# Performance work log

Hardware: AMD Instinct MI355X
Metric: run time of the kernel (lower is better)

The kernel has to match this reference:

```python
import jax, jax.numpy as jnp
import numpy as np

B = 65536          # batch
E = 512            # embedding_dim
SL = 128           # speed_latent_dim
H = 256            # hidden_size
NB = 6             # num_branch
D = E + SL         # 640, branch input dim


def _linear_init(k, din, dout):
    bound = 1.0 / np.sqrt(din)
    kw, kb = jax.random.split(k)
    W = jax.random.uniform(kw, (din, dout), minval=-bound, maxval=bound, dtype=jnp.float32)
    b = jax.random.uniform(kb, (dout,), minval=-bound, maxval=bound, dtype=jnp.float32)
    return W, b


def setup_inputs() -> dict:
    key = jax.random.key(0)
    ks = jax.random.split(key, 10)
    embedding = jax.random.normal(ks[0], (B, E), dtype=jnp.float32)
    speed = jax.random.uniform(ks[1], (B, 1), dtype=jnp.float32)
    command = jax.random.randint(ks[2], (B,), 1, NB + 1)  # values in 1..6

    # speed_in: Linear(1,H) -> ReLU -> Linear(H,SL)
    si_W1, si_b1 = _linear_init(ks[3], 1, H)
    si_W2, si_b2 = _linear_init(ks[4], H, SL)

    # speed_out: Linear(D,H) -> ReLU -> Linear(H,H) -> ReLU -> Linear(H,1)
    so_W1, so_b1 = _linear_init(ks[5], D, H)
    so_W2, so_b2 = _linear_init(ks[6], H, H)
    so_W3, so_b3 = _linear_init(ks[7], H, 1)

    # NB branches, each Linear(D,H)->ReLU->Linear(H,H)->ReLU->Linear(H,3)->Sigmoid
    def mk_branch(k):
        k1, k2, k3 = jax.random.split(k, 3)
        W1, b1 = _linear_init(k1, D, H)
        W2, b2 = _linear_init(k2, H, H)
        W3, b3 = _linear_init(k3, H, 3)
        return W1, b1, W2, b2, W3, b3

    bW1, bb1, bW2, bb2, bW3, bb3 = jax.vmap(mk_branch)(jax.random.split(ks[8], NB))

    return {
        "embedding": embedding, "speed": speed, "command": command,
        "si_W1": si_W1, "si_b1": si_b1, "si_W2": si_W2, "si_b2": si_b2,
        "bW1": bW1, "bb1": bb1, "bW2": bW2, "bb2": bb2, "bW3": bW3, "bb3": bb3,
        "so_W1": so_W1, "so_b1": so_b1, "so_W2": so_W2, "so_b2": so_b2,
        "so_W3": so_W3, "so_b3": so_b3,
    }


def reference(embedding, speed, command,
              si_W1, si_b1, si_W2, si_b2,
              bW1, bb1, bW2, bb2, bW3, bb3,
              so_W1, so_b1, so_W2, so_b2, so_W3, so_b3):
    # speed_in MLP and concat
    s = jax.nn.relu(speed @ si_W1 + si_b1) @ si_W2 + si_b2          # [B, SL]
    emb = jnp.concatenate([embedding, s], axis=1)                    # [B, D]

    # all branches computed densely (as in the torch module), then one-hot mask
    h1 = jax.nn.relu(jnp.einsum('bd,ndh->nbh', emb, bW1) + bb1[:, None, :])   # [NB,B,H]
    h2 = jax.nn.relu(jnp.einsum('nbh,nhk->nbk', h1, bW2) + bb2[:, None, :])   # [NB,B,H]
    out = jax.nn.sigmoid(jnp.einsum('nbk,nko->nbo', h2, bW3) + bb3[:, None, :])  # [NB,B,3]

    mask = (jnp.arange(NB)[:, None] == (command - 1)[None, :]).astype(out.dtype)  # [NB,B]
    control_pred = jnp.sum(out * mask[:, :, None], axis=0)           # [B, 3]

    # speed prediction head
    sp = jax.nn.relu(emb @ so_W1 + so_b1)
    sp = jax.nn.relu(sp @ so_W2 + so_b2)
    speed_pred = sp @ so_W3 + so_b3                                  # [B, 1]

    return control_pred, speed_pred
```

## Files before the change

kernel.cpp:

```cpp
#include <hip/hip_runtime.h>
#include <cstdint>
#include <cstddef>

typedef _Float16 f16;
typedef f16 f16x8 __attribute__((ext_vector_type(8)));
typedef float f32x4 __attribute__((ext_vector_type(4)));

#define B_ROWS 65536
#define TILE_M 128
#define NT_BRANCH 518
#define NT_SPEED 512
#define NWG_HEADS (NT_BRANCH + NT_SPEED)

constexpr size_t OFF_AF16   = 0;
constexpr size_t SZ_AF16    = (size_t)B_ROWS * 640 * 2;
constexpr size_t OFF_SIW2T  = OFF_AF16 + SZ_AF16;
constexpr size_t SZ_SIW2T   = (size_t)128 * 256 * 2;
constexpr size_t OFF_BW1T   = OFF_SIW2T + SZ_SIW2T;
constexpr size_t SZ_BW1T    = (size_t)6 * 256 * 640 * 2;
constexpr size_t OFF_BW2T   = OFF_BW1T + SZ_BW1T;
constexpr size_t SZ_BW2T    = (size_t)6 * 256 * 256 * 2;
constexpr size_t OFF_SOW1T  = OFF_BW2T + SZ_BW2T;
constexpr size_t SZ_SOW1T   = (size_t)256 * 640 * 2;
constexpr size_t OFF_SOW2T  = OFF_SOW1T + SZ_SOW1T;
constexpr size_t SZ_SOW2T   = (size_t)256 * 256 * 2;
constexpr size_t OFF_BW3T16 = OFF_SOW2T + SZ_SOW2T;
constexpr size_t SZ_BW3T16  = (size_t)6 * 16 * 256 * 2;
constexpr size_t OFF_SOW3T16= OFF_BW3T16 + SZ_BW3T16;
constexpr size_t SZ_SOW3T16 = (size_t)16 * 256 * 2;
constexpr size_t OFF_COUNTS = OFF_SOW3T16 + SZ_SOW3T16;
constexpr size_t OFF_CURSORS= OFF_COUNTS + 256;
constexpr size_t OFF_BINBASE= OFF_CURSORS + 256;
constexpr size_t OFF_TILECMD= OFF_BINBASE + 256;
constexpr size_t OFF_PERM   = OFF_TILECMD + 4352;
constexpr size_t WS_NEEDED  = OFF_PERM + (size_t)NT_BRANCH * TILE_M * 4;

#define MFMA16(a, b, c) __builtin_amdgcn_mfma_f32_16x16x32_f16(a, b, c, 0, 0, 0)
#define BARSYNC() asm volatile("s_waitcnt lgkmcnt(0)\n\ts_barrier" ::: "memory")

__global__ void prep_kernel(const float* __restrict__ emb,
                            const float* __restrict__ siW2,
                            const float* __restrict__ bW1,
                            const float* __restrict__ bW2,
                            const float* __restrict__ soW1,
                            const float* __restrict__ soW2,
                            const float* __restrict__ bW3,
                            const float* __restrict__ soW3,
                            f16* __restrict__ AF16,
                            f16* __restrict__ siW2T, f16* __restrict__ bW1T,
                            f16* __restrict__ bW2T, f16* __restrict__ soW1T,
                            f16* __restrict__ soW2T,
                            f16* __restrict__ bW3T16, f16* __restrict__ soW3T16,
                            int* __restrict__ counts, int* __restrict__ cursors,
                            int* __restrict__ perm)
{
    const int bx = blockIdx.x;
    const int tx = threadIdx.x, ty = threadIdx.y;
    const int tid = ty * 32 + tx;
    if (bx >= 1860) {
        const int cb = bx - 1860;
        const int wv = tid >> 6, ln = tid & 63;
        #pragma unroll
        for (int it = 0; it < 4; ++it) {
            const int row = cb * 16 + it * 4 + wv;
            const float* src = emb + (size_t)row * 512 + ln * 8;
            const float4 f0 = ((const float4*)src)[0];
            const float4 f1 = ((const float4*)src)[1];
            f16x8 v;
            v[0] = (f16)f0.x; v[1] = (f16)f0.y; v[2] = (f16)f0.z; v[3] = (f16)f0.w;
            v[4] = (f16)f1.x; v[5] = (f16)f1.y; v[6] = (f16)f1.z; v[7] = (f16)f1.w;
            *(f16x8*)(AF16 + (size_t)row * 640 + ln * 8) = v;
        }
        return;
    }
    if (bx >= 1601) {
        const int ib = bx - 1601;
        const int idx = ib * 256 + tid;
        if (idx < NT_BRANCH * TILE_M) perm[idx] = -1;
        if (ib == 0 && tid < 6) { counts[tid] = 0; cursors[tid] = 0; }
        return;
    }
    if (bx == 1600) {
        for (int i = tid; i < 6 * 16 * 256; i += 256) {
            const int c = i >> 12, rem = i & 4095, n = rem >> 8, k = rem & 255;
            bW3T16[i] = (n < 3) ? (f16)bW3[((size_t)c * 256 + k) * 3 + n] : (f16)0;
        }
        for (int i = tid; i < 16 * 256; i += 256) {
            const int n = i >> 8, k = i & 255;
            soW3T16[i] = (n == 0) ? (f16)soW3[k] : (f16)0;
        }
        return;
    }
    const float* in; f16* out; int R, C, lb;
    if (bx < 960)       { int m = bx / 160;        lb = bx - m * 160;       in = bW1 + (size_t)m * 640 * 256; out = bW1T + (size_t)m * 640 * 256; R = 640; C = 256; }
    else if (bx < 1344) { int m = (bx - 960) / 64; lb = (bx - 960) - m * 64; in = bW2 + (size_t)m * 256 * 256; out = bW2T + (size_t)m * 256 * 256; R = 256; C = 256; }
    else if (bx < 1504) { lb = bx - 1344; in = soW1; out = soW1T; R = 640; C = 256; }
    else if (bx < 1568) { lb = bx - 1504; in = soW2; out = soW2T; R = 256; C = 256; }
    else                { lb = bx - 1568; in = siW2; out = siW2T; R = 256; C = 128; }
    const int txt = C >> 5;
    const int c0 = (lb % txt) << 5;
    const int r0 = (lb / txt) << 5;
    __shared__ float tile[32][33];
    #pragma unroll
    for (int i = 0; i < 4; ++i)
        tile[tx][ty + 8 * i] = in[(size_t)(r0 + ty + 8 * i) * C + c0 + tx];
    __syncthreads();
    #pragma unroll
    for (int i = 0; i < 4; ++i)
        out[(size_t)(c0 + ty + 8 * i) * R + r0 + tx] = (f16)tile[ty + 8 * i][tx];
}

__global__ __launch_bounds__(256) void speedin_kernel(
    const float* __restrict__ speed,
    const float* __restrict__ siW1, const float* __restrict__ sib1,
    const f16* __restrict__ siW2T, const float* __restrict__ sib2,
    const int* __restrict__ cmd,
    f16* __restrict__ AF16, int* __restrict__ counts)
{
    __shared__ f16 H[64 * 264];
    __shared__ float spd[64];
    __shared__ int h[6];
    const int tid = threadIdx.x;
    const int rb = blockIdx.x * 64;
    if (tid < 6) h[tid] = 0;
    __syncthreads();
    if (tid < 64) {
        spd[tid] = speed[rb + tid];
        atomicAdd(&h[cmd[rb + tid] - 1], 1);
    }
    __syncthreads();
    if (tid < 6 && h[tid] > 0) atomicAdd(&counts[tid], h[tid]);
    {
        const float w1 = siW1[tid], b1v = sib1[tid];
        #pragma unroll 4
        for (int r = 0; r < 64; ++r) {
            float hv = spd[r] * w1 + b1v;
            H[r * 264 + tid] = (f16)(hv > 0.f ? hv : 0.f);
        }
    }
    __syncthreads();
    const int w = tid >> 6, lane = tid & 63, lq = lane >> 4, l16 = lane & 15;
    const int nb = w * 32;
    f32x4 acc[4][2];
    #pragma unroll
    for (int mt = 0; mt < 4; ++mt)
        #pragma unroll
        for (int nt = 0; nt < 2; ++nt)
            acc[mt][nt] = (f32x4){0.f, 0.f, 0.f, 0.f};
    for (int ks = 0; ks < 8; ++ks) {
        const int koff = ks * 32 + lq * 8;
        f16x8 af[4], bf[2];
        #pragma unroll
        for (int mt = 0; mt < 4; ++mt)
            af[mt] = *(const f16x8*)(&H[(mt * 16 + l16) * 264 + koff]);
        #pragma unroll
        for (int nt = 0; nt < 2; ++nt)
            bf[nt] = *(const f16x8*)(siW2T + (size_t)(nb + nt * 16 + l16) * 256 + koff);
        #pragma unroll
        for (int mt = 0; mt < 4; ++mt)
            #pragma unroll
            for (int nt = 0; nt < 2; ++nt)
                acc[mt][nt] = MFMA16(af[mt], bf[nt], acc[mt][nt]);
    }
    #pragma unroll
    for (int mt = 0; mt < 4; ++mt)
        #pragma unroll
        for (int nt = 0; nt < 2; ++nt) {
            const int n = nb + nt * 16 + l16;
            const float bv = sib2[n];
            #pragma unroll
            for (int r2 = 0; r2 < 4; ++r2) {
                const int m = mt * 16 + lq * 4 + r2;
                AF16[(size_t)(rb + m) * 640 + 512 + n] = (f16)(acc[mt][nt][r2] + bv);
            }
        }
}

__global__ void plan_kernel(const int* __restrict__ counts,
                            int* __restrict__ binBase, int* __restrict__ tile_cmd) {
    __shared__ int tbase[7];
    if (threadIdx.x == 0) {
        int base = 0, tb = 0;
        for (int c = 0; c < 6; ++c) {
            binBase[c] = base;
            tbase[c] = tb;
            const int nt = (counts[c] + TILE_M - 1) >> 7;
            tb += nt;
            base += nt << 7;
        }
        tbase[6] = tb;
    }
    __syncthreads();
    for (int t = threadIdx.x; t < NT_BRANCH; t += 256) {
        int c = -1;
        #pragma unroll
        for (int j = 0; j < 6; ++j)
            if (t >= tbase[j] && t < tbase[j + 1]) c = j;
        tile_cmd[t] = c;
    }
}

__global__ void place_kernel(const int* __restrict__ cmd,
                             const int* __restrict__ binBase,
                             int* __restrict__ cursors, int* __restrict__ perm) {
    __shared__ int lcnt[6], lbase[6];
    const int tid = threadIdx.x;
    if (tid < 6) lcnt[tid] = 0;
    __syncthreads();
    const int i = blockIdx.x * 256 + tid;
    const int c = cmd[i] - 1;
    const int myr = atomicAdd(&lcnt[c], 1);
    __syncthreads();
    if (tid < 6) lbase[tid] = atomicAdd(&cursors[tid], lcnt[tid]);
    __syncthreads();
    perm[binBase[c] + lbase[c] + myr] = i;
}

__global__ __launch_bounds__(512, 3) void heads_kernel(
    const f16* __restrict__ AF16,
    const int* __restrict__ perm, const int* __restrict__ tile_cmd,
    const f16* __restrict__ bW1T, const f16* __restrict__ bW2T,
    const f16* __restrict__ bW3T16,
    const float* __restrict__ bb1, const float* __restrict__ bb2,
    const float* __restrict__ bb3,
    const f16* __restrict__ soW1T, const f16* __restrict__ soW2T,
    const f16* __restrict__ soW3T16,
    const float* __restrict__ sob1, const float* __restrict__ sob2,
    const float* __restrict__ sob3,
    float* __restrict__ out)
{
    __shared__ f16 smem[33792];
    __shared__ int rowIdx[TILE_M];
    const int orig = blockIdx.x;
    const int xcd = orig & 7, idx = orig >> 3;
    constexpr int q = NWG_HEADS >> 3, rr = NWG_HEADS & 7;
    const int bx = (xcd < rr ? xcd * (q + 1) : rr * (q + 1) + (xcd - rr) * q) + idx;
    const int tid = threadIdx.x;
    const bool is_speed = (bx >= NT_BRANCH);
    const f16 *W1T, *W2T, *W3T;
    const float *bias1, *bias2, *bias3;
    if (is_speed) {
        const int t = bx - NT_BRANCH;
        if (tid < TILE_M) rowIdx[tid] = t * TILE_M + tid;
        W1T = soW1T; W2T = soW2T; W3T = soW3T16;
        bias1 = sob1; bias2 = sob2; bias3 = sob3;
    } else {
        const int c = tile_cmd[bx];
        if (c < 0) return;
        if (tid < TILE_M) rowIdx[tid] = perm[bx * TILE_M + tid];
        W1T = bW1T + (size_t)c * 256 * 640;
        W2T = bW2T + (size_t)c * 256 * 256;
        W3T = bW3T16 + (size_t)c * 16 * 256;
        bias1 = bb1 + c * 256; bias2 = bb2 + c * 256; bias3 = bb3 + c * 3;
    }
    __syncthreads();

    const int r = tid >> 2, p = tid & 3;
    int growS = rowIdx[r]; if (growS < 0) growS = 0;
    const f16* srcA = AF16 + (size_t)growS * 640 + p * 16;
    const int pOff = r * 72 + p * 16;

    const int w = tid >> 6, lane = tid & 63, lq = lane >> 4, l16 = lane & 15;
    const int nb = w * 32;
    const f16* brow0 = W1T + (size_t)(nb + l16) * 640;
    const f16* brow1 = W1T + (size_t)(nb + 16 + l16) * 640;

    f32x4 acc[8][2];
    #pragma unroll
    for (int mt = 0; mt < 8; ++mt)
        #pragma unroll
        for (int nt = 0; nt < 2; ++nt)
            acc[mt][nt] = (f32x4){0.f, 0.f, 0.f, 0.f};

    f16x8 sreg[4][2];
    #pragma unroll
    for (int j = 0; j < 4; ++j) {
        sreg[j][0] = ((const f16x8*)(srcA + j * 64))[0];
        sreg[j][1] = ((const f16x8*)(srcA + j * 64))[1];
    }
    f16x8 Bb[2][2];
    #pragma unroll
    for (int ks = 0; ks < 2; ++ks) {
        Bb[ks][0] = *(const f16x8*)(brow0 + ks * 32 + lq * 8);
        Bb[ks][1] = *(const f16x8*)(brow1 + ks * 32 + lq * 8);
    }
    *(f16x8*)(smem + pOff) = sreg[0][0];
    *(f16x8*)(smem + pOff + 8) = sreg[0][1];
    BARSYNC();

    #pragma unroll
    for (int kc = 0; kc < 10; ++kc) {
        const f16* cur = smem + (kc & 1) * 9216;
        if (kc < 9) {
            f16* dst = smem + ((kc + 1) & 1) * 9216 + pOff;
            *(f16x8*)(dst)     = sreg[(kc + 1) & 3][0];
            *(f16x8*)(dst + 8) = sreg[(kc + 1) & 3][1];
        }
        if (kc < 6) {
            sreg[kc & 3][0] = ((const f16x8*)(srcA + (kc + 4) * 64))[0];
            sreg[kc & 3][1] = ((const f16x8*)(srcA + (kc + 4) * 64))[1];
        }
        f16x8 Bn[2][2];
        if (kc < 9) {
            #pragma unroll
            for (int ks = 0; ks < 2; ++ks) {
                Bn[ks][0] = *(const f16x8*)(brow0 + (kc + 1) * 64 + ks * 32 + lq * 8);
                Bn[ks][1] = *(const f16x8*)(brow1 + (kc + 1) * 64 + ks * 32 + lq * 8);
            }
        }
        #pragma unroll
        for (int ks = 0; ks < 2; ++ks)
            #pragma unroll
            for (int mh = 0; mh < 2; ++mh) {
                f16x8 a[4];
                #pragma unroll
                for (int mt = 0; mt < 4; ++mt)
                    a[mt] = *(const f16x8*)(cur + ((mh * 4 + mt) * 16 + l16) * 72 + ks * 32 + lq * 8);
                #pragma unroll
                for (int mt = 0; mt < 4; ++mt) {
                    acc[mh * 4 + mt][0] = MFMA16(a[mt], Bb[ks][0], acc[mh * 4 + mt][0]);
                    acc[mh * 4 + mt][1] = MFMA16(a[mt], Bb[ks][1], acc[mh * 4 + mt][1]);
                }
            }
        if (kc < 9) {
            #pragma unroll
            for (int ks = 0; ks < 2; ++ks)
                #pragma unroll
                for (int nt = 0; nt < 2; ++nt)
                    Bb[ks][nt] = Bn[ks][nt];
        }
        BARSYNC();
    }

    const f16* brow2[2];
    #pragma unroll
    for (int nt = 0; nt < 2; ++nt)
        brow2[nt] = W2T + (size_t)(nb + nt * 16 + l16) * 256;
    f16x8 Bd[2][2];
    #pragma unroll
    for (int nt = 0; nt < 2; ++nt)
        Bd[0][nt] = *(const f16x8*)(brow2[nt] + lq * 8);

    #pragma unroll
    for (int mt = 0; mt < 8; ++mt)
        #pragma unroll
        for (int nt = 0; nt < 2; ++nt) {
            const int n = nb + nt * 16 + l16;
            const float bv = bias1[n];
            #pragma unroll
            for (int r2 = 0; r2 < 4; ++r2) {
                const int m = mt * 16 + lq * 4 + r2;
                const float v = acc[mt][nt][r2] + bv;
                smem[m * 264 + n] = (f16)(v > 0.f ? v : 0.f);
            }
            acc[mt][nt] = (f32x4){0.f, 0.f, 0.f, 0.f};
        }
    BARSYNC();

    #pragma unroll
    for (int ks = 0; ks < 8; ++ks) {
        if (ks < 7) {
            #pragma unroll
            for (int nt = 0; nt < 2; ++nt)
                Bd[(ks + 1) & 1][nt] = *(const f16x8*)(brow2[nt] + (ks + 1) * 32 + lq * 8);
        }
        #pragma unroll
        for (int mh = 0; mh < 2; ++mh) {
            f16x8 a[4];
            #pragma unroll
            for (int mt = 0; mt < 4; ++mt)
                a[mt] = *(const f16x8*)(&smem[((mh * 4 + mt) * 16 + l16) * 264 + ks * 32 + lq * 8]);
            #pragma unroll
            for (int mt = 0; mt < 4; ++mt) {
                acc[mh * 4 + mt][0] = MFMA16(a[mt], Bd[ks & 1][0], acc[mh * 4 + mt][0]);
                acc[mh * 4 + mt][1] = MFMA16(a[mt], Bd[ks & 1][1], acc[mh * 4 + mt][1]);
            }
        }
    }
    BARSYNC();
    #pragma unroll
    for (int mt = 0; mt < 8; ++mt)
        #pragma unroll
        for (int nt = 0; nt < 2; ++nt) {
            const int n = nb + nt * 16 + l16;
            const float bv = bias2[n];
            #pragma unroll
            for (int r2 = 0; r2 < 4; ++r2) {
                const int m = mt * 16 + lq * 4 + r2;
                const float v = acc[mt][nt][r2] + bv;
                smem[m * 264 + n] = (f16)(v > 0.f ? v : 0.f);
            }
        }
    BARSYNC();
    {
        f32x4 acc3 = (f32x4){0.f, 0.f, 0.f, 0.f};
        const f16* w3row = W3T + (size_t)l16 * 256;
        #pragma unroll
        for (int ks = 0; ks < 8; ++ks) {
            const int koff = ks * 32 + lq * 8;
            const f16x8 af = *(const f16x8*)(&smem[(w * 16 + l16) * 264 + koff]);
            const f16x8 bf = *(const f16x8*)(w3row + koff);
            acc3 = MFMA16(af, bf, acc3);
        }
        const int orow = w * 16 + lq * 4;
        if (!is_speed) {
            if (l16 < 3) {
                const float b3 = bias3[l16];
                #pragma unroll
                for (int r2 = 0; r2 < 4; ++r2) {
                    const int g = rowIdx[orow + r2];
                    if (g >= 0)
                        out[(size_t)g * 3 + l16] = 1.f / (1.f + __expf(-(acc3[r2] + b3)));
                }
            }
        } else {
            if (l16 == 0) {
                const float b3 = bias3[0];
                #pragma unroll
                for (int r2 = 0; r2 < 4; ++r2) {
                    const int g = rowIdx[orow + r2];
                    if (g >= 0)
                        out[(size_t)3 * B_ROWS + g] = acc3[r2] + b3;
                }
            }
        }
    }
}

extern "C" void kernel_launch(void* const* d_in, const int* in_sizes, int n_in,
                              void* d_out, int out_size, void* d_ws, size_t ws_size,
                              hipStream_t stream) {
    (void)in_sizes; (void)n_in; (void)out_size; (void)ws_size;
    const float* embedding = (const float*)d_in[0];
    const float* speed     = (const float*)d_in[1];
    const int*   command   = (const int*)d_in[2];
    const float* si_W1 = (const float*)d_in[3];
    const float* si_b1 = (const float*)d_in[4];
    const float* si_W2 = (const float*)d_in[5];
    const float* si_b2 = (const float*)d_in[6];
    const float* bW1   = (const float*)d_in[7];
    const float* bb1   = (const float*)d_in[8];
    const float* bW2   = (const float*)d_in[9];
    const float* bb2   = (const float*)d_in[10];
    const float* bW3   = (const float*)d_in[11];
    const float* bb3   = (const float*)d_in[12];
    const float* so_W1 = (const float*)d_in[13];
    const float* so_b1 = (const float*)d_in[14];
    const float* so_W2 = (const float*)d_in[15];
    const float* so_b2 = (const float*)d_in[16];
    const float* so_W3 = (const float*)d_in[17];
    const float* so_b3 = (const float*)d_in[18];
    float* out = (float*)d_out;

    char* ws = (char*)d_ws;
    f16* AF16   = (f16*)(ws + OFF_AF16);
    f16* siW2T  = (f16*)(ws + OFF_SIW2T);
    f16* bW1T   = (f16*)(ws + OFF_BW1T);
    f16* bW2T   = (f16*)(ws + OFF_BW2T);
    f16* soW1T  = (f16*)(ws + OFF_SOW1T);
    f16* soW2T  = (f16*)(ws + OFF_SOW2T);
    f16* bW3T16 = (f16*)(ws + OFF_BW3T16);
    f16* soW3T16= (f16*)(ws + OFF_SOW3T16);
    int* counts = (int*)(ws + OFF_COUNTS);
    int* cursors= (int*)(ws + OFF_CURSORS);
    int* binBase= (int*)(ws + OFF_BINBASE);
    int* tile_cmd = (int*)(ws + OFF_TILECMD);
    int* perm   = (int*)(ws + OFF_PERM);

    prep_kernel<<<1860 + 4096, dim3(32, 8), 0, stream>>>(
        embedding, si_W2, bW1, bW2, so_W1, so_W2, bW3, so_W3,
        AF16, siW2T, bW1T, bW2T, soW1T, soW2T, bW3T16, soW3T16,
        counts, cursors, perm);
    speedin_kernel<<<1024, 256, 0, stream>>>(
        speed, si_W1, si_b1, siW2T, si_b2, command, AF16, counts);
    plan_kernel<<<1, 256, 0, stream>>>(counts, binBase, tile_cmd);
    place_kernel<<<256, 256, 0, stream>>>(command, binBase, cursors, perm);
    heads_kernel<<<NWG_HEADS, 512, 0, stream>>>(
        AF16, perm, tile_cmd,
        bW1T, bW2T, bW3T16, bb1, bb2, bb3,
        soW1T, soW2T, soW3T16, so_b1, so_b2, so_b3, out);
}
```

Measured before the change: 378.9 us.

## Fuse speed-in MLP into heads kernel and fold command histogram into prep

Removes the separate speedin and plan kernels. Each heads workgroup now computes the speed-latent MLP for its own 128 rows in shared memory and feeds it as the last two K-chunks of the first GEMM, instead of reading them from AF16. Command counts become per-block partials written by prep and reduced redundantly inside every place_kernel block, which also builds tile_cmd. The XCD-aware block remapping is dropped. Launch count and AF16 traffic go down, but every branch tile recomputes the speed MLP, branch tiles now recompute rather than share it, and shared memory use grows.

```diff
diff --git a/kernel.cpp b/kernel.cpp
--- a/kernel.cpp
+++ b/kernel.cpp
@@ -11,6 +11,7 @@
 #define NT_BRANCH 518
 #define NT_SPEED 512
 #define NWG_HEADS (NT_BRANCH + NT_SPEED)
+#define NCVT 4096
 
 constexpr size_t OFF_AF16   = 0;
 constexpr size_t SZ_AF16    = (size_t)B_ROWS * 640 * 2;
@@ -28,10 +29,10 @@
 constexpr size_t SZ_BW3T16  = (size_t)6 * 16 * 256 * 2;
 constexpr size_t OFF_SOW3T16= OFF_BW3T16 + SZ_BW3T16;
 constexpr size_t SZ_SOW3T16 = (size_t)16 * 256 * 2;
-constexpr size_t OFF_COUNTS = OFF_SOW3T16 + SZ_SOW3T16;
-constexpr size_t OFF_CURSORS= OFF_COUNTS + 256;
-constexpr size_t OFF_BINBASE= OFF_CURSORS + 256;
-constexpr size_t OFF_TILECMD= OFF_BINBASE + 256;
+constexpr size_t OFF_PART   = OFF_SOW3T16 + SZ_SOW3T16;
+constexpr size_t SZ_PART    = (size_t)NCVT * 6 * 4;
+constexpr size_t OFF_CURSORS= OFF_PART + SZ_PART;
+constexpr size_t OFF_TILECMD= OFF_CURSORS + 256;
 constexpr size_t OFF_PERM   = OFF_TILECMD + 4352;
 constexpr size_t WS_NEEDED  = OFF_PERM + (size_t)NT_BRANCH * TILE_M * 4;
 
@@ -39,6 +40,7 @@
 #define BARSYNC() asm volatile("s_waitcnt lgkmcnt(0)\n\ts_barrier" ::: "memory")
 
 __global__ void prep_kernel(const float* __restrict__ emb,
+                            const int* __restrict__ cmd,
                             const float* __restrict__ siW2,
                             const float* __restrict__ bW1,
                             const float* __restrict__ bW2,
@@ -51,7 +53,7 @@
                             f16* __restrict__ bW2T, f16* __restrict__ soW1T,
                             f16* __restrict__ soW2T,
                             f16* __restrict__ bW3T16, f16* __restrict__ soW3T16,
-                            int* __restrict__ counts, int* __restrict__ cursors,
+                            int* __restrict__ partials, int* __restrict__ cursors,
                             int* __restrict__ perm)
 {
     const int bx = blockIdx.x;
@@ -59,6 +61,10 @@
     const int tid = ty * 32 + tx;
     if (bx >= 1860) {
         const int cb = bx - 1860;
+        __shared__ int lc[6];
+        if (tid < 6) lc[tid] = 0;
+        __syncthreads();
+        if (tid < 16) atomicAdd(&lc[cmd[cb * 16 + tid] - 1], 1);
         const int wv = tid >> 6, ln = tid & 63;
         #pragma unroll
         for (int it = 0; it < 4; ++it) {
@@ -71,13 +77,15 @@
             v[4] = (f16)f1.x; v[5] = (f16)f1.y; v[6] = (f16)f1.z; v[7] = (f16)f1.w;
             *(f16x8*)(AF16 + (size_t)row * 640 + ln * 8) = v;
         }
+        __syncthreads();
+        if (tid < 6) partials[cb * 6 + tid] = lc[tid];
         return;
     }
     if (bx >= 1601) {
         const int ib = bx - 1601;
         const int idx = ib * 256 + tid;
         if (idx < NT_BRANCH * TILE_M) perm[idx] = -1;
-        if (ib == 0 && tid < 6) { counts[tid] = 0; cursors[tid] = 0; }
+        if (ib == 0 && tid < 6) cursors[tid] = 0;
         return;
     }
     if (bx == 1600) {
@@ -110,114 +118,58 @@
         out[(size_t)(c0 + ty + 8 * i) * R + r0 + tx] = (f16)tile[ty + 8 * i][tx];
 }
 
-__global__ __launch_bounds__(256) void speedin_kernel(
-    const float* __restrict__ speed,
-    const float* __restrict__ siW1, const float* __restrict__ sib1,
-    const f16* __restrict__ siW2T, const float* __restrict__ sib2,
-    const int* __restrict__ cmd,
-    f16* __restrict__ AF16, int* __restrict__ counts)
-{
-    __shared__ f16 H[64 * 264];
-    __shared__ float spd[64];
-    __shared__ int h[6];
-    const int tid = threadIdx.x;
-    const int rb = blockIdx.x * 64;
-    if (tid < 6) h[tid] = 0;
-    __syncthreads();
-    if (tid < 64) {
-        spd[tid] = speed[rb + tid];
-        atomicAdd(&h[cmd[rb + tid] - 1], 1);
-    }
-    __syncthreads();
-    if (tid < 6 && h[tid] > 0) atomicAdd(&counts[tid], h[tid]);
-    {
-        const float w1 = siW1[tid], b1v = sib1[tid];
-        #pragma unroll 4
-        for (int r = 0; r < 64; ++r) {
-            float hv = spd[r] * w1 + b1v;
-            H[r * 264 + tid] = (f16)(hv > 0.f ? hv : 0.f);
-        }
-    }
-    __syncthreads();
-    const int w = tid >> 6, lane = tid & 63, lq = lane >> 4, l16 = lane & 15;
-    const int nb = w * 32;
-    f32x4 acc[4][2];
-    #pragma unroll
-    for (int mt = 0; mt < 4; ++mt)
-        #pragma unroll
-        for (int nt = 0; nt < 2; ++nt)
-            acc[mt][nt] = (f32x4){0.f, 0.f, 0.f, 0.f};
-    for (int ks = 0; ks < 8; ++ks) {
-        const int koff = ks * 32 + lq * 8;
-        f16x8 af[4], bf[2];
-        #pragma unroll
-        for (int mt = 0; mt < 4; ++mt)
-            af[mt] = *(const f16x8*)(&H[(mt * 16 + l16) * 264 + koff]);
-        #pragma unroll
-        for (int nt = 0; nt < 2; ++nt)
-            bf[nt] = *(const f16x8*)(siW2T + (size_t)(nb + nt * 16 + l16) * 256 + koff);
-        #pragma unroll
-        for (int mt = 0; mt < 4; ++mt)
-            #pragma unroll
-            for (int nt = 0; nt < 2; ++nt)
-                acc[mt][nt] = MFMA16(af[mt], bf[nt], acc[mt][nt]);
-    }
-    #pragma unroll
-    for (int mt = 0; mt < 4; ++mt)
-        #pragma unroll
-        for (int nt = 0; nt < 2; ++nt) {
-            const int n = nb + nt * 16 + l16;
-            const float bv = sib2[n];
-            #pragma unroll
-            for (int r2 = 0; r2 < 4; ++r2) {
-                const int m = mt * 16 + lq * 4 + r2;
-                AF16[(size_t)(rb + m) * 640 + 512 + n] = (f16)(acc[mt][nt][r2] + bv);
-            }
-        }
-}
-
-__global__ void plan_kernel(const int* __restrict__ counts,
-                            int* __restrict__ binBase, int* __restrict__ tile_cmd) {
-    __shared__ int tbase[7];
-    if (threadIdx.x == 0) {
-        int base = 0, tb = 0;
-        for (int c = 0; c < 6; ++c) {
-            binBase[c] = base;
-            tbase[c] = tb;
-            const int nt = (counts[c] + TILE_M - 1) >> 7;
-            tb += nt;
-            base += nt << 7;
-        }
-        tbase[6] = tb;
-    }
-    __syncthreads();
-    for (int t = threadIdx.x; t < NT_BRANCH; t += 256) {
-        int c = -1;
-        #pragma unroll
-        for (int j = 0; j < 6; ++j)
-            if (t >= tbase[j] && t < tbase[j + 1]) c = j;
-        tile_cmd[t] = c;
-    }
-}
-
-__global__ void place_kernel(const int* __restrict__ cmd,
-                             const int* __restrict__ binBase,
-                             int* __restrict__ cursors, int* __restrict__ perm) {
+__global__ __launch_bounds__(256) void place_kernel(const int* __restrict__ cmd,
+                             const int* __restrict__ partials,
+                             int* __restrict__ cursors, int* __restrict__ perm,
+                             int* __restrict__ tile_cmd) {
+    __shared__ int shc[6];
     __shared__ int lcnt[6], lbase[6];
     const int tid = threadIdx.x;
-    if (tid < 6) lcnt[tid] = 0;
+    if (tid < 6) { shc[tid] = 0; lcnt[tid] = 0; }
     __syncthreads();
+    int loc[6] = {0, 0, 0, 0, 0, 0};
+    for (int i = tid; i < NCVT; i += 256) {
+        #pragma unroll
+        for (int c = 0; c < 6; ++c) loc[c] += partials[i * 6 + c];
+    }
+    #pragma unroll
+    for (int c = 0; c < 6; ++c)
+        if (loc[c]) atomicAdd(&shc[c], loc[c]);
+    __syncthreads();
+    int binB[6], tb[7];
+    {
+        int base = 0, t = 0;
+        #pragma unroll
+        for (int c = 0; c < 6; ++c) {
+            binB[c] = base; tb[c] = t;
+            const int nt = (shc[c] + TILE_M - 1) >> 7;
+            t += nt; base += nt << 7;
+        }
+        tb[6] = t;
+    }
+    if (blockIdx.x == 0) {
+        for (int t = tid; t < NT_BRANCH; t += 256) {
+            int c = -1;
+            #pragma unroll
+            for (int j = 0; j < 6; ++j)
+                if (t >= tb[j] && t < tb[j + 1]) c = j;
+            tile_cmd[t] = c;
+        }
+    }
     const int i = blockIdx.x * 256 + tid;
     const int c = cmd[i] - 1;
     const int myr = atomicAdd(&lcnt[c], 1);
     __syncthreads();
     if (tid < 6) lbase[tid] = atomicAdd(&cursors[tid], lcnt[tid]);
     __syncthreads();
-    perm[binBase[c] + lbase[c] + myr] = i;
+    perm[binB[c] + lbase[c] + myr] = i;
 }
 
 __global__ __launch_bounds__(512, 3) void heads_kernel(
     const f16* __restrict__ AF16,
+    const float* __restrict__ speed,
+    const float* __restrict__ siW1, const float* __restrict__ sib1,
+    const f16* __restrict__ siW2T, const float* __restrict__ sib2,
     const int* __restrict__ perm, const int* __restrict__ tile_cmd,
     const f16* __restrict__ bW1T, const f16* __restrict__ bW2T,
     const f16* __restrict__ bW3T16,
@@ -229,25 +181,31 @@
     const float* __restrict__ sob3,
     float* __restrict__ out)
 {
-    __shared__ f16 smem[33792];
+    __shared__ f16 smem[35840];
+    __shared__ float spd[TILE_M];
     __shared__ int rowIdx[TILE_M];
-    const int orig = blockIdx.x;
-    const int xcd = orig & 7, idx = orig >> 3;
-    constexpr int q = NWG_HEADS >> 3, rr = NWG_HEADS & 7;
-    const int bx = (xcd < rr ? xcd * (q + 1) : rr * (q + 1) + (xcd - rr) * q) + idx;
+    const int bx = blockIdx.x;
     const int tid = threadIdx.x;
     const bool is_speed = (bx >= NT_BRANCH);
     const f16 *W1T, *W2T, *W3T;
     const float *bias1, *bias2, *bias3;
     if (is_speed) {
         const int t = bx - NT_BRANCH;
-        if (tid < TILE_M) rowIdx[tid] = t * TILE_M + tid;
+        if (tid < TILE_M) {
+            const int g = t * TILE_M + tid;
+            rowIdx[tid] = g;
+            spd[tid] = speed[g];
+        }
         W1T = soW1T; W2T = soW2T; W3T = soW3T16;
         bias1 = sob1; bias2 = sob2; bias3 = sob3;
     } else {
         const int c = tile_cmd[bx];
         if (c < 0) return;
-        if (tid < TILE_M) rowIdx[tid] = perm[bx * TILE_M + tid];
+        if (tid < TILE_M) {
+            const int g = perm[bx * TILE_M + tid];
+            rowIdx[tid] = g;
+            spd[tid] = speed[g < 0 ? 0 : g];
+        }
         W1T = bW1T + (size_t)c * 256 * 640;
         W2T = bW2T + (size_t)c * 256 * 256;
         W3T = bW3T16 + (size_t)c * 16 * 256;
@@ -262,22 +220,75 @@
 
     const int w = tid >> 6, lane = tid & 63, lq = lane >> 4, l16 = lane & 15;
     const int nb = w * 32;
-    const f16* brow0 = W1T + (size_t)(nb + l16) * 640;
-    const f16* brow1 = W1T + (size_t)(nb + 16 + l16) * 640;
-
-    f32x4 acc[8][2];
-    #pragma unroll
-    for (int mt = 0; mt < 8; ++mt)
-        #pragma unroll
-        for (int nt = 0; nt < 2; ++nt)
-            acc[mt][nt] = (f32x4){0.f, 0.f, 0.f, 0.f};
-
+
+    {
+        const int hr = tid >> 2, kb = (tid & 3) * 64;
+        const float sv = spd[hr];
+        #pragma unroll
+        for (int j = 0; j < 8; ++j) {
+            const float4 w0 = *(const float4*)(siW1 + kb + j * 8);
+            const float4 w1 = *(const float4*)(siW1 + kb + j * 8 + 4);
+            const float4 b0 = *(const float4*)(sib1 + kb + j * 8);
+            const float4 b1 = *(const float4*)(sib1 + kb + j * 8 + 4);
+            float t0 = sv * w0.x + b0.x, t1 = sv * w0.y + b0.y;
+            float t2 = sv * w0.z + b0.z, t3 = sv * w0.w + b0.w;
+            float t4 = sv * w1.x + b1.x, t5 = sv * w1.y + b1.y;
+            float t6 = sv * w1.z + b1.z, t7 = sv * w1.w + b1.w;
+            f16x8 hv;
+            hv[0] = (f16)(t0 > 0.f ? t0 : 0.f); hv[1] = (f16)(t1 > 0.f ? t1 : 0.f);
+            hv[2] = (f16)(t2 > 0.f ? t2 : 0.f); hv[3] = (f16)(t3 > 0.f ? t3 : 0.f);
+            hv[4] = (f16)(t4 > 0.f ? t4 : 0.f); hv[5] = (f16)(t5 > 0.f ? t5 : 0.f);
+            hv[6] = (f16)(t6 > 0.f ? t6 : 0.f); hv[7] = (f16)(t7 > 0.f ? t7 : 0.f);
+            *(f16x8*)(smem + hr * 264 + kb + j * 8) = hv;
+        }
+    }
     f16x8 sreg[4][2];
     #pragma unroll
     for (int j = 0; j < 4; ++j) {
         sreg[j][0] = ((const f16x8*)(srcA + j * 64))[0];
         sreg[j][1] = ((const f16x8*)(srcA + j * 64))[1];
     }
+    BARSYNC();
+
+    {
+        const int mrb = (w >> 2) * 64, ncb = (w & 3) * 32;
+        const f16* w2r0 = siW2T + (size_t)(ncb + l16) * 256;
+        const f16* w2r1 = siW2T + (size_t)(ncb + 16 + l16) * 256;
+        f32x4 accs[4][2];
+        #pragma unroll
+        for (int mt = 0; mt < 4; ++mt)
+            #pragma unroll
+            for (int nt = 0; nt < 2; ++nt)
+                accs[mt][nt] = (f32x4){0.f, 0.f, 0.f, 0.f};
+        #pragma unroll
+        for (int ks = 0; ks < 8; ++ks) {
+            const int koff = ks * 32 + lq * 8;
+            const f16x8 bf0 = *(const f16x8*)(w2r0 + koff);
+            const f16x8 bf1 = *(const f16x8*)(w2r1 + koff);
+            #pragma unroll
+            for (int mt = 0; mt < 4; ++mt) {
+                const f16x8 af = *(const f16x8*)(&smem[(mrb + mt * 16 + l16) * 264 + koff]);
+                accs[mt][0] = MFMA16(af, bf0, accs[mt][0]);
+                accs[mt][1] = MFMA16(af, bf1, accs[mt][1]);
+            }
+        }
+        BARSYNC();
+        #pragma unroll
+        for (int nt = 0; nt < 2; ++nt) {
+            const int n = ncb + nt * 16 + l16;
+            const float sb = sib2[n];
+            #pragma unroll
+            for (int mt = 0; mt < 4; ++mt)
+                #pragma unroll
+                for (int r2 = 0; r2 < 4; ++r2) {
+                    const int m = mrb + mt * 16 + lq * 4 + r2;
+                    smem[18432 + m * 136 + n] = (f16)(accs[mt][nt][r2] + sb);
+                }
+        }
+    }
+
+    const f16* brow0 = W1T + (size_t)(nb + l16) * 640;
+    const f16* brow1 = W1T + (size_t)(nb + 16 + l16) * 640;
     f16x8 Bb[2][2];
     #pragma unroll
     for (int ks = 0; ks < 2; ++ks) {
@@ -286,17 +297,24 @@
     }
     *(f16x8*)(smem + pOff) = sreg[0][0];
     *(f16x8*)(smem + pOff + 8) = sreg[0][1];
+
+    f32x4 acc[8][2];
+    #pragma unroll
+    for (int mt = 0; mt < 8; ++mt)
+        #pragma unroll
+        for (int nt = 0; nt < 2; ++nt)
+            acc[mt][nt] = (f32x4){0.f, 0.f, 0.f, 0.f};
     BARSYNC();
 
     #pragma unroll
     for (int kc = 0; kc < 10; ++kc) {
         const f16* cur = smem + (kc & 1) * 9216;
-        if (kc < 9) {
+        if (kc < 7) {
             f16* dst = smem + ((kc + 1) & 1) * 9216 + pOff;
             *(f16x8*)(dst)     = sreg[(kc + 1) & 3][0];
             *(f16x8*)(dst + 8) = sreg[(kc + 1) & 3][1];
         }
-        if (kc < 6) {
+        if (kc < 4) {
             sreg[kc & 3][0] = ((const f16x8*)(srcA + (kc + 4) * 64))[0];
             sreg[kc & 3][1] = ((const f16x8*)(srcA + (kc + 4) * 64))[1];
         }
@@ -314,8 +332,12 @@
             for (int mh = 0; mh < 2; ++mh) {
                 f16x8 a[4];
                 #pragma unroll
-                for (int mt = 0; mt < 4; ++mt)
-                    a[mt] = *(const f16x8*)(cur + ((mh * 4 + mt) * 16 + l16) * 72 + ks * 32 + lq * 8);
+                for (int mt = 0; mt < 4; ++mt) {
+                    const int row = (mh * 4 + mt) * 16 + l16;
+                    a[mt] = (kc < 8)
+                        ? *(const f16x8*)(cur + row * 72 + ks * 32 + lq * 8)
+                        : *(const f16x8*)(smem + 18432 + row * 136 + (kc - 8) * 64 + ks * 32 + lq * 8);
+                }
                 #pragma unroll
                 for (int mt = 0; mt < 4; ++mt) {
                     acc[mh * 4 + mt][0] = MFMA16(a[mt], Bb[ks][0], acc[mh * 4 + mt][0]);
@@ -461,22 +483,19 @@
     f16* soW2T  = (f16*)(ws + OFF_SOW2T);
     f16* bW3T16 = (f16*)(ws + OFF_BW3T16);
     f16* soW3T16= (f16*)(ws + OFF_SOW3T16);
-    int* counts = (int*)(ws + OFF_COUNTS);
-    int* cursors= (int*)(ws + OFF_CURSORS);
-    int* binBase= (int*)(ws + OFF_BINBASE);
+    int* partials = (int*)(ws + OFF_PART);
+    int* cursors  = (int*)(ws + OFF_CURSORS);
     int* tile_cmd = (int*)(ws + OFF_TILECMD);
-    int* perm   = (int*)(ws + OFF_PERM);
-
-    prep_kernel<<<1860 + 4096, dim3(32, 8), 0, stream>>>(
-        embedding, si_W2, bW1, bW2, so_W1, so_W2, bW3, so_W3,
+    int* perm     = (int*)(ws + OFF_PERM);
+
+    prep_kernel<<<1860 + NCVT, dim3(32, 8), 0, stream>>>(
+        embedding, command, si_W2, bW1, bW2, so_W1, so_W2, bW3, so_W3,
         AF16, siW2T, bW1T, bW2T, soW1T, soW2T, bW3T16, soW3T16,
-        counts, cursors, perm);
-    speedin_kernel<<<1024, 256, 0, stream>>>(
-        speed, si_W1, si_b1, siW2T, si_b2, command, AF16, counts);
-    plan_kernel<<<1, 256, 0, stream>>>(counts, binBase, tile_cmd);
-    place_kernel<<<256, 256, 0, stream>>>(command, binBase, cursors, perm);
+        partials, cursors, perm);
+    place_kernel<<<256, 256, 0, stream>>>(command, partials, cursors, perm, tile_cmd);
     heads_kernel<<<NWG_HEADS, 512, 0, stream>>>(
-        AF16, perm, tile_cmd,
+        AF16, speed, si_W1, si_b1, siW2T, si_b2,
+        perm, tile_cmd,
         bW1T, bW2T, bW3T16, bb1, bb2, bb3,
         soW1T, soW2T, soW3T16, so_b1, so_b2, so_b3, out);
 }
```

New measurement: 418.3 us. 10.4% more time.
